# Optimization experiments

Hardware: AMD Instinct MI355X
Metric: run time of the kernel (lower is better)

Reference implementation:

```python
import jax, jax.numpy as jnp
import numpy as np

B, N, D2, S = 64, 4096, 128, 512  # b, n, 2*d, size_s


def setup_inputs() -> dict:
    key = jax.random.key(0)
    k1, k2, k3, k4 = jax.random.split(key, 4)
    s_past = jax.random.randint(k1, (B, N), 0, S)
    yq = jax.random.normal(k2, (B, 1, D2), dtype=jnp.float32)
    y_past = jax.random.normal(k3, (B, N, D2), dtype=jnp.float32)
    w_mat = jax.random.normal(k4, (D2, D2), dtype=jnp.float32)
    return {"s_past": s_past, "yq": yq, "y_past": y_past, "w_mat": w_mat, "size_s": S}


def reference(s_past, yq, y_past, w_mat, size_s):
    # attn_logits[b,n] = yq[b,0,:] @ w_mat @ y_past[b,n,:]
    attn_logits = jnp.einsum('bqd,de,bne->bn', yq, w_mat, y_past)
    attn = jax.nn.softmax(attn_logits, axis=-1)  # (b, n)
    b, n = s_past.shape
    # post_est[b, s] = sum_n attn[b, n] * [s_past[b, n] == s]
    # fused scatter-add instead of materializing one-hot (b, n, S)
    flat_ids = (s_past + size_s * jnp.arange(b, dtype=s_past.dtype)[:, None]).reshape(-1)
    post_est = jax.ops.segment_sum(attn.reshape(-1), flat_ids,
                                   num_segments=b * size_s).reshape(b, size_s)
    return post_est
```

## Files before the change

### kernel.cpp

```cpp
#include <hip/hip_runtime.h>
#include <math.h>

#define BB 64
#define NN 4096
#define DD 128
#define SS 512

template <int CH>
__global__ __launch_bounds__(256) void fused_kernel(
    const float* __restrict__ y_past, const float* __restrict__ yq,
    const float* __restrict__ w, const int* __restrict__ s_past,
    float* __restrict__ bins_g, float* __restrict__ pmax) {
    constexpr int RPC  = NN / CH;
    constexpr int SUBT = RPC / 64;
    const int b = blockIdx.x, chunk = blockIdx.y;
    const int t = threadIdx.x;
    const int j = t & 3;
    const int r = t >> 2;

    __shared__ float qsh[DD];
    __shared__ float bins[SS];
    __shared__ float wred[4];

    const float4* gp =
        (const float4*)y_past + ((size_t)b * NN + (size_t)chunk * RPC) * 32;

    float4 y0[4];
#pragma unroll
    for (int k = 0; k < 4; ++k) y0[k] = gp[(size_t)r * 32 + j * 8 + k];

    int sreg[SUBT];
    if (j == 0) {
#pragma unroll
        for (int s = 0; s < SUBT; ++s)
            sreg[s] = s_past[(size_t)b * NN + chunk * RPC + s * 64 + r];
    }

    bins[t] = 0.f;
    bins[t + 256] = 0.f;

    if (t < DD) {
        const float* yqb = yq + b * DD;
        float acc = 0.f;
#pragma unroll
        for (int d = 0; d < DD; ++d) acc = fmaf(yqb[d], w[d * DD + t], acc);
        qsh[t] = acc;
    }

    __syncthreads();

    float4 qreg[8];
#pragma unroll
    for (int k = 0; k < 8; ++k) qreg[k] = ((const float4*)qsh)[j * 8 + k];

    float pv[SUBT];

    {
        float4 acc = {0.f, 0.f, 0.f, 0.f};
#pragma unroll
        for (int k = 0; k < 4; ++k) {
            acc.x = fmaf(qreg[k].x, y0[k].x, acc.x);
            acc.y = fmaf(qreg[k].y, y0[k].y, acc.y);
            acc.z = fmaf(qreg[k].z, y0[k].z, acc.z);
            acc.w = fmaf(qreg[k].w, y0[k].w, acc.w);
        }
#pragma unroll
        for (int k = 4; k < 8; ++k) {
            float4 yv = gp[(size_t)r * 32 + j * 8 + k];
            acc.x = fmaf(qreg[k].x, yv.x, acc.x);
            acc.y = fmaf(qreg[k].y, yv.y, acc.y);
            acc.z = fmaf(qreg[k].z, yv.z, acc.z);
            acc.w = fmaf(qreg[k].w, yv.w, acc.w);
        }
        float p = (acc.x + acc.y) + (acc.z + acc.w);
        p += __shfl_xor(p, 1, 64);
        p += __shfl_xor(p, 2, 64);
        pv[0] = p;
    }

#pragma unroll
    for (int s = 1; s < SUBT; ++s) {
        float4 acc = {0.f, 0.f, 0.f, 0.f};
#pragma unroll
        for (int k = 0; k < 8; ++k) {
            float4 yv = gp[(size_t)(s * 64 + r) * 32 + j * 8 + k];
            acc.x = fmaf(qreg[k].x, yv.x, acc.x);
            acc.y = fmaf(qreg[k].y, yv.y, acc.y);
            acc.z = fmaf(qreg[k].z, yv.z, acc.z);
            acc.w = fmaf(qreg[k].w, yv.w, acc.w);
        }
        float p = (acc.x + acc.y) + (acc.z + acc.w);
        p += __shfl_xor(p, 1, 64);
        p += __shfl_xor(p, 2, 64);
        pv[s] = p;
    }

    float m = pv[0];
#pragma unroll
    for (int s = 1; s < SUBT; ++s) m = fmaxf(m, pv[s]);
#pragma unroll
    for (int off = 32; off > 0; off >>= 1) m = fmaxf(m, __shfl_xor(m, off, 64));
    const int wave = t >> 6, lane = t & 63;
    if (lane == 0) wred[wave] = m;
    __syncthreads();
    m = fmaxf(fmaxf(wred[0], wred[1]), fmaxf(wred[2], wred[3]));

    if (j == 0) {
#pragma unroll
        for (int s = 0; s < SUBT; ++s)
            atomicAdd(&bins[sreg[s]], __expf(pv[s] - m));
    }
    __syncthreads();

    float* bg = bins_g + ((size_t)b * CH + chunk) * SS;
    bg[t] = bins[t];
    bg[t + 256] = bins[t + 256];
    if (t == 0) pmax[b * CH + chunk] = m;
}

template <int CH>
__global__ __launch_bounds__(512) void combine_kernel(
    const float* __restrict__ bins_g, const float* __restrict__ pmax,
    float* __restrict__ out) {
    int b = blockIdx.x;
    int t = threadIdx.x;
    __shared__ float scale[CH];
    __shared__ float red[8];
    __shared__ float sInv;

    if (t < CH) scale[t] = pmax[b * CH + t];
    __syncthreads();
    if (t == 0) {
        float M = scale[0];
#pragma unroll
        for (int c = 1; c < CH; ++c) M = fmaxf(M, scale[c]);
#pragma unroll
        for (int c = 0; c < CH; ++c) scale[c] = __expf(scale[c] - M);
    }
    __syncthreads();

    float acc = 0.f;
#pragma unroll
    for (int c = 0; c < CH; ++c)
        acc = fmaf(bins_g[((size_t)b * CH + c) * SS + t], scale[c], acc);

    float s = acc;
#pragma unroll
    for (int off = 32; off > 0; off >>= 1) s += __shfl_xor(s, off, 64);
    if ((t & 63) == 0) red[t >> 6] = s;
    __syncthreads();
    if (t == 0) {
        float S = 0.f;
#pragma unroll
        for (int i = 0; i < 8; ++i) S += red[i];
        sInv = 1.f / S;
    }
    __syncthreads();

    out[b * SS + t] = acc * sInv;
}

extern "C" void kernel_launch(void* const* d_in, const int* in_sizes, int n_in,
                              void* d_out, int out_size, void* d_ws, size_t ws_size,
                              hipStream_t stream) {
    const int*   s_past = (const int*)d_in[0];
    const float* yq     = (const float*)d_in[1];
    const float* y_past = (const float*)d_in[2];
    const float* w_mat  = (const float*)d_in[3];

    float* ws  = (float*)d_ws;
    float* out = (float*)d_out;

    const size_t need32 =
        ((size_t)BB * 32 * SS + (size_t)BB * 32) * sizeof(float);

    if (ws_size >= need32) {
        float* bins_g = ws;
        float* pmax   = bins_g + (size_t)BB * 32 * SS;
        fused_kernel<32><<<dim3(BB, 32), 256, 0, stream>>>(
            y_past, yq, w_mat, s_past, bins_g, pmax);
        combine_kernel<32><<<BB, SS, 0, stream>>>(bins_g, pmax, out);
    } else {
        float* bins_g = ws;
        float* pmax   = bins_g + (size_t)BB * 16 * SS;
        fused_kernel<16><<<dim3(BB, 16), 256, 0, stream>>>(
            y_past, yq, w_mat, s_past, bins_g, pmax);
        combine_kernel<16><<<BB, SS, 0, stream>>>(bins_g, pmax, out);
    }
}
```

Before: 208.1 us.

## Coalesce y_past loads per wave with transpose-style shuffle reduction

Each wave now reads contiguous float4 runs of y_past (lane-contiguous), so global loads are fully coalesced. It software-prefetches the next tile while reducing, and folds eight partial dot products per lane through a butterfly exchange so each shuffle carries useful data. Row logits go to shared memory, and the exp and atomic bin scatter run once per row with all threads. The raw s_barrier after an lgkmcnt wait replaces __syncthreads, and the change adds shared memory and register pressure.

```diff
diff --git a/kernel.cpp b/kernel.cpp
--- a/kernel.cpp
+++ b/kernel.cpp
@@ -11,30 +11,28 @@
     const float* __restrict__ y_past, const float* __restrict__ yq,
     const float* __restrict__ w, const int* __restrict__ s_past,
     float* __restrict__ bins_g, float* __restrict__ pmax) {
-    constexpr int RPC  = NN / CH;
-    constexpr int SUBT = RPC / 64;
+    constexpr int RPC = NN / CH;
+    constexpr int RPW = RPC / 4;
+    constexpr int NT  = RPW / 16;
     const int b = blockIdx.x, chunk = blockIdx.y;
     const int t = threadIdx.x;
-    const int j = t & 3;
-    const int r = t >> 2;
+    const int l = t & 63, wav = t >> 6;
 
     __shared__ float qsh[DD];
+    __shared__ float rowtot[RPC];
     __shared__ float bins[SS];
     __shared__ float wred[4];
 
-    const float4* gp =
-        (const float4*)y_past + ((size_t)b * NN + (size_t)chunk * RPC) * 32;
+    const float4* gp4 =
+        (const float4*)y_past + ((size_t)b * NN + (size_t)chunk * RPC) * (DD / 4);
+    const int waveBase = wav * RPW * (DD / 4);
 
-    float4 y0[4];
+    float4 yv[8];
 #pragma unroll
-    for (int k = 0; k < 4; ++k) y0[k] = gp[(size_t)r * 32 + j * 8 + k];
+    for (int k = 0; k < 8; ++k) yv[k] = gp4[waveBase + k * 64 + l];
 
-    int sreg[SUBT];
-    if (j == 0) {
-#pragma unroll
-        for (int s = 0; s < SUBT; ++s)
-            sreg[s] = s_past[(size_t)b * NN + chunk * RPC + s * 64 + r];
-    }
+    int sidx = 0;
+    if (t < RPC) sidx = s_past[(size_t)b * NN + chunk * RPC + t];
 
     bins[t] = 0.f;
     bins[t + 256] = 0.f;
@@ -46,70 +44,67 @@
         for (int d = 0; d < DD; ++d) acc = fmaf(yqb[d], w[d * DD + t], acc);
         qsh[t] = acc;
     }
+    asm volatile("s_waitcnt lgkmcnt(0)" ::: "memory");
+    __builtin_amdgcn_s_barrier();
 
-    __syncthreads();
+    const float4 q4 = ((const float4*)qsh)[l & 31];
+    const bool g4 = (l & 4) != 0, g2 = (l & 2) != 0, g1 = (l & 1) != 0;
+    float mloc = -1e30f;
 
-    float4 qreg[8];
 #pragma unroll
-    for (int k = 0; k < 8; ++k) qreg[k] = ((const float4*)qsh)[j * 8 + k];
-
-    float pv[SUBT];
-
-    {
-        float4 acc = {0.f, 0.f, 0.f, 0.f};
+    for (int T = 0; T < NT; ++T) {
+        float a[8];
+#pragma unroll
+        for (int k = 0; k < 8; ++k) {
+            float4 y = yv[k];
+            float s = y.x * q4.x;
+            s = fmaf(y.y, q4.y, s);
+            s = fmaf(y.z, q4.z, s);
+            s = fmaf(y.w, q4.w, s);
+            a[k] = s;
+        }
+        if (T + 1 < NT) {
+#pragma unroll
+            for (int k = 0; k < 8; ++k)
+                yv[k] = gp4[waveBase + (T + 1) * 512 + k * 64 + l];
+        }
+#pragma unroll
+        for (int k = 0; k < 8; ++k) a[k] += __shfl_xor(a[k], 16, 64);
+#pragma unroll
+        for (int k = 0; k < 8; ++k) a[k] += __shfl_xor(a[k], 8, 64);
+        float b4[4];
 #pragma unroll
         for (int k = 0; k < 4; ++k) {
-            acc.x = fmaf(qreg[k].x, y0[k].x, acc.x);
-            acc.y = fmaf(qreg[k].y, y0[k].y, acc.y);
-            acc.z = fmaf(qreg[k].z, y0[k].z, acc.z);
-            acc.w = fmaf(qreg[k].w, y0[k].w, acc.w);
+            float send = g4 ? a[k] : a[k + 4];
+            float keep = g4 ? a[k + 4] : a[k];
+            b4[k] = keep + __shfl_xor(send, 4, 64);
         }
+        float b2[2];
 #pragma unroll
-        for (int k = 4; k < 8; ++k) {
-            float4 yv = gp[(size_t)r * 32 + j * 8 + k];
-            acc.x = fmaf(qreg[k].x, yv.x, acc.x);
-            acc.y = fmaf(qreg[k].y, yv.y, acc.y);
-            acc.z = fmaf(qreg[k].z, yv.z, acc.z);
-            acc.w = fmaf(qreg[k].w, yv.w, acc.w);
+        for (int k = 0; k < 2; ++k) {
+            float send = g2 ? b4[k] : b4[k + 2];
+            float keep = g2 ? b4[k + 2] : b4[k];
+            b2[k] = keep + __shfl_xor(send, 2, 64);
         }
-        float p = (acc.x + acc.y) + (acc.z + acc.w);
-        p += __shfl_xor(p, 1, 64);
-        p += __shfl_xor(p, 2, 64);
-        pv[0] = p;
+        {
+            float send = g1 ? b2[0] : b2[1];
+            float keep = g1 ? b2[1] : b2[0];
+            float tot = keep + __shfl_xor(send, 1, 64);
+            if ((l & 31) < 8)
+                rowtot[wav * RPW + T * 16 + 2 * (l & 7) + (l >> 5)] = tot;
+            mloc = fmaxf(mloc, tot);
+        }
     }
 
 #pragma unroll
-    for (int s = 1; s < SUBT; ++s) {
-        float4 acc = {0.f, 0.f, 0.f, 0.f};
-#pragma unroll
-        for (int k = 0; k < 8; ++k) {
-            float4 yv = gp[(size_t)(s * 64 + r) * 32 + j * 8 + k];
-            acc.x = fmaf(qreg[k].x, yv.x, acc.x);
-            acc.y = fmaf(qreg[k].y, yv.y, acc.y);
-            acc.z = fmaf(qreg[k].z, yv.z, acc.z);
-            acc.w = fmaf(qreg[k].w, yv.w, acc.w);
-        }
-        float p = (acc.x + acc.y) + (acc.z + acc.w);
-        p += __shfl_xor(p, 1, 64);
-        p += __shfl_xor(p, 2, 64);
-        pv[s] = p;
-    }
+    for (int off = 32; off > 0; off >>= 1)
+        mloc = fmaxf(mloc, __shfl_xor(mloc, off, 64));
+    if (l == 0) wred[wav] = mloc;
+    asm volatile("s_waitcnt lgkmcnt(0)" ::: "memory");
+    __builtin_amdgcn_s_barrier();
+    const float m = fmaxf(fmaxf(wred[0], wred[1]), fmaxf(wred[2], wred[3]));
 
-    float m = pv[0];
-#pragma unroll
-    for (int s = 1; s < SUBT; ++s) m = fmaxf(m, pv[s]);
-#pragma unroll
-    for (int off = 32; off > 0; off >>= 1) m = fmaxf(m, __shfl_xor(m, off, 64));
-    const int wave = t >> 6, lane = t & 63;
-    if (lane == 0) wred[wave] = m;
-    __syncthreads();
-    m = fmaxf(fmaxf(wred[0], wred[1]), fmaxf(wred[2], wred[3]));
-
-    if (j == 0) {
-#pragma unroll
-        for (int s = 0; s < SUBT; ++s)
-            atomicAdd(&bins[sreg[s]], __expf(pv[s] - m));
-    }
+    if (t < RPC) atomicAdd(&bins[sidx], __expf(rowtot[t] - m));
     __syncthreads();
 
     float* bg = bins_g + ((size_t)b * CH + chunk) * SS;
```

New measurement: 205.3 us. No clear change (-1.3%).
